# Kernel optimization log

Measured on AMD Instinct MI355X. Metric: run time of the kernel, lower is better.

The kernel has to match this reference:

```python
import jax, jax.numpy as jnp
import numpy as np
from jax import lax

B, C, H, W, E = 16, 256, 64, 64, 4
KH = KW = 3
EPS = 1e-5  # torch BatchNorm2d default


def conv2d(x, w, groups=1):
    # x: [N, Cin, H, W], w: [Cout, Cin/groups, KH, KW], stride 1, pad 1 (autopad for k=3)
    return lax.conv_general_dilated(
        x, w, window_strides=(1, 1), padding=[(1, 1), (1, 1)],
        dimension_numbers=('NCHW', 'OIHW', 'NCHW'),
        feature_group_count=groups)


def bn(t, g, b, m, v):
    # eval-mode batchnorm over channel dim of [N, C, H, W]
    scale = g / jnp.sqrt(v + EPS)
    return (t - m[:, None, None]) * scale[:, None, None] + b[:, None, None]


def silu(t):
    return t * jax.nn.sigmoid(t)


def setup_inputs() -> dict:
    key = jax.random.key(0)
    ks = jax.random.split(key, 8)
    s = lambda k, sh: jax.random.normal(k, sh, jnp.float32) * 0.05
    return {
        'x': jax.random.normal(ks[0], (B, C, H, W), jnp.float32),
        # cv1: Conv(c1, c_, 3) = conv(no bias) + BN + SiLU
        'w1': s(ks[1], (C, C, KH, KW)),
        'bn1_g': jnp.ones((C,), jnp.float32),
        'bn1_b': jnp.zeros((C,), jnp.float32),
        'bn1_m': s(ks[2], (C,)),
        'bn1_v': jnp.abs(s(ks[3], (C,))) + 1.0,
        # cv2: DynamicConv routing linear (C -> E experts)
        'wr': s(ks[4], (E, C)),
        'br': jnp.zeros((E,), jnp.float32),
        # CondConv2d expert weight bank: [E, Cout*Cin*KH*KW]
        'w_e': s(ks[5], (E, C * C * KH * KW)),
        # cv2 BatchNorm2d
        'bn2_g': jnp.ones((C,), jnp.float32),
        'bn2_b': jnp.zeros((C,), jnp.float32),
        'bn2_m': s(ks[6], (C,)),
        'bn2_v': jnp.abs(s(ks[7], (C,))) + 1.0,
    }


def reference(x, w1, bn1_g, bn1_b, bn1_m, bn1_v, wr, br, w_e,
              bn2_g, bn2_b, bn2_m, bn2_v):
    # cv1: standard YOLO Conv (3x3, pad 1) + BN + SiLU
    y = silu(bn(conv2d(x, w1), bn1_g, bn1_b, bn1_m, bn1_v))  # [B, C, H, W]

    # DynamicConv_Single: global-avg-pool routing -> sigmoid gates over experts
    pooled = y.mean(axis=(2, 3))                       # [B, C]
    routing = jax.nn.sigmoid(pooled @ wr.T + br)       # [B, E]

    # CondConv2d: per-sample expert-weighted kernel, applied via batch-as-groups
    kern = (routing @ w_e).reshape(B * C, C, KH, KW)   # [B*Cout, Cin, 3, 3]
    yc = conv2d(y.reshape(1, B * C, H, W), kern, groups=B).reshape(B, C, H, W)

    # cv2 BN + SiLU, then residual add (shortcut and c1 == c2)
    out = silu(bn(yc, bn2_g, bn2_b, bn2_m, bn2_v))
    return x + out


if __name__ == '__main__':
    o = reference(**setup_inputs())
    print(o.shape, o.dtype)
```

## Files before the change

### kernel.cpp

```cpp
#include <hip/hip_runtime.h>
#include <math.h>

typedef _Float16 h16;
typedef _Float16 half8 __attribute__((ext_vector_type(8)));
typedef float f32x4 __attribute__((ext_vector_type(4)));

#define BATCH 16
#define CH 256
#define EPSBN 1e-5f

constexpr size_t WE_STRIDE = (size_t)CH * CH * 9;
constexpr int RSTRIDE = 2120;
constexpr int BUFH    = 4 * RSTRIDE;

__device__ __forceinline__ float silu_(float v) {
    return v * (1.0f / (1.0f + __expf(-v)));
}

template<int MODE>
__global__ __launch_bounds__(256, 4)
void conv_mfma(const h16* __restrict__ xin,
               const h16* __restrict__ wt,
               const float* __restrict__ bng, const float* __restrict__ bnb,
               const float* __restrict__ bnm, const float* __restrict__ bnv,
               const float* __restrict__ resid,
               void* __restrict__ outv)
{
    __shared__ h16 xt[2 * BUFH];

    const int t = threadIdx.x;
    const int swz = (blockIdx.x & 7) * 128 + (blockIdx.x >> 3);
    const int bx  = swz & 31;
    const int gy  = swz >> 5;
    const int by  = gy & 1;
    const int bz  = gy >> 1;
    const int h0  = bx * 2;
    const int co0 = by * 128;
    const int wv   = t >> 6;
    const int ws   = wv >> 1;
    const int wc   = wv & 1;
    const int lane = t & 63;
    const int quad = lane >> 4;
    const int l15  = lane & 15;

    f32x4 acc[16];
    #pragma unroll
    for (int i = 0; i < 16; ++i) {
        f32x4 z = {0.f, 0.f, 0.f, 0.f};
        acc[i] = z;
    }

    const h16* wrow = wt + ((MODE == 1) ? (size_t)bz * 9 * 65536 : (size_t)0)
                         + ((size_t)(co0 + wc * 64 + l15) << 8)
                         + (size_t)(quad * 8);

    const h16* xb = xin + ((size_t)bz << 20);
    int goff[5];
    #pragma unroll
    for (int k = 0; k < 5; ++k) {
        int slot = k * 64 + lane;
        int row = slot / 66;
        int col = slot - row * 66;
        int gh = h0 - 1 + row, gw = col - 1;
        goff[k] = -1;
        if (slot < 264 && (unsigned)gh < 64u && (unsigned)gw < 64u)
            goff[k] = ((gh << 6) + gw) * 256 + wv * 8;
    }

    {
        half8 z = {0, 0, 0, 0, 0, 0, 0, 0};
        #pragma unroll
        for (int k = 0; k < 5; ++k) {
            int slot = k * 64 + lane;
            if (slot < 264 && goff[k] < 0) {
                *(half8*)(xt + wv * RSTRIDE + slot * 8) = z;
                *(half8*)(xt + BUFH + wv * RSTRIDE + slot * 8) = z;
            }
        }
    }

    auto stage = [&](int b, int ci0) {
        const h16* g = xb + ci0;
        #pragma unroll
        for (int k = 0; k < 5; ++k) {
            if (goff[k] >= 0)
                __builtin_amdgcn_global_load_lds(
                    (const __attribute__((address_space(1))) void*)(g + goff[k]),
                    (__attribute__((address_space(3))) void*)(xt + b * BUFH + wv * RSTRIDE + k * 512),
                    16, 0, 0);
        }
    };

    stage(0, 0);
    __syncthreads();

    for (int c = 0; c < 8; ++c) {
        if (c < 7) stage((c + 1) & 1, (c + 1) * 32);

        const h16* xq  = xt + (c & 1) * BUFH + quad * RSTRIDE + l15 * 8;
        const h16* wcp = wrow + c * 32;
        #pragma unroll
        for (int kh = 0; kh < 3; ++kh)
        #pragma unroll
        for (int kw = 0; kw < 3; ++kw) {
            const int tap = kh * 3 + kw;
            half8 wf[4], xf[4];
            #pragma unroll
            for (int f = 0; f < 4; ++f)
                wf[f] = *(const half8*)(wcp + (size_t)tap * 65536 + f * 4096);
            #pragma unroll
            for (int i = 0; i < 4; ++i)
                xf[i] = *(const half8*)(xq + ((ws + kh) * 66 + i * 16 + kw) * 8);
            if (MODE == 0) {
                #pragma unroll
                for (int i = 0; i < 4; ++i)
                    #pragma unroll
                    for (int j = 0; j < 4; ++j)
                        acc[i * 4 + j] = __builtin_amdgcn_mfma_f32_16x16x32_f16(
                            xf[i], wf[j], acc[i * 4 + j], 0, 0, 0);
            } else {
                #pragma unroll
                for (int i = 0; i < 4; ++i)
                    #pragma unroll
                    for (int j = 0; j < 4; ++j)
                        acc[i * 4 + j] = __builtin_amdgcn_mfma_f32_16x16x32_f16(
                            wf[i], xf[j], acc[i * 4 + j], 0, 0, 0);
            }
        }
        __syncthreads();
    }

    if (MODE == 0) {
        h16* yout = (h16*)outv;
        float sc[4], sh[4];
        #pragma unroll
        for (int j = 0; j < 4; ++j) {
            int cch = co0 + wc * 64 + j * 16 + l15;
            float s = bng[cch] * rsqrtf(bnv[cch] + EPSBN);
            sc[j] = s; sh[j] = bnb[cch] - bnm[cch] * s;
        }
        const int h = h0 + ws;
        #pragma unroll
        for (int i = 0; i < 4; ++i)
            #pragma unroll
            for (int r = 0; r < 4; ++r) {
                int w = i * 16 + quad * 4 + r;
                size_t base = (((size_t)(bz * 64 + h) << 6) + w) * 256
                            + co0 + wc * 64 + l15;
                #pragma unroll
                for (int j = 0; j < 4; ++j) {
                    float v = acc[i * 4 + j][r] * sc[j] + sh[j];
                    yout[base + j * 16] = (h16)silu_(v);
                }
            }
    } else {
        h16* ycp = (h16*)outv;
        const int h = h0 + ws;
        #pragma unroll
        for (int i = 0; i < 4; ++i) {
            float sc[4], sh[4];
            #pragma unroll
            for (int r = 0; r < 4; ++r) {
                int cch = co0 + wc * 64 + i * 16 + quad * 4 + r;
                float s = bng[cch] * rsqrtf(bnv[cch] + EPSBN);
                sc[r] = s; sh[r] = bnb[cch] - bnm[cch] * s;
            }
            #pragma unroll
            for (int j = 0; j < 4; ++j) {
                int w = j * 16 + l15;
                #pragma unroll
                for (int r = 0; r < 4; ++r) {
                    int cch = co0 + wc * 64 + i * 16 + quad * 4 + r;
                    size_t idx = ((size_t)(bz * CH + cch) << 12) + (h << 6) + w;
                    float v = acc[i * 4 + j][r] * sc[r] + sh[r];
                    ycp[idx] = (h16)silu_(v);
                }
            }
        }
    }
}

__global__ __launch_bounds__(256)
void finalize_kernel(const h16* __restrict__ yc, const float* __restrict__ x,
                     float* __restrict__ out) {
    const int total8 = BATCH * CH * 4096 / 8;
    int i = blockIdx.x * 256 + threadIdx.x;
    const int stride = gridDim.x * 256;
    for (; i < total8; i += stride) {
        half8 v = *(const half8*)(yc + (size_t)i * 8);
        const float4* xp = (const float4*)(x + (size_t)i * 8);
        float4 a = xp[0], b = xp[1];
        float4 o0, o1;
        o0.x = a.x + (float)v[0];
        o0.y = a.y + (float)v[1];
        o0.z = a.z + (float)v[2];
        o0.w = a.w + (float)v[3];
        o1.x = b.x + (float)v[4];
        o1.y = b.y + (float)v[5];
        o1.z = b.z + (float)v[6];
        o1.w = b.w + (float)v[7];
        float4* op = (float4*)(out + (size_t)i * 8);
        op[0] = o0;
        op[1] = o1;
    }
}

__global__ __launch_bounds__(256)
void prep_x(const float* __restrict__ x, h16* __restrict__ xh) {
    __shared__ float lt[64][65];
    int cg = blockIdx.x, h = blockIdx.y, b = blockIdx.z;
    int t = threadIdx.x;
    {
        int cl = t >> 2, wq = t & 3;
        const float4* src = (const float4*)(x + (((size_t)(b * CH + cg * 64 + cl)) << 12)
                                              + ((size_t)h << 6));
        #pragma unroll
        for (int k = 0; k < 4; ++k) {
            int w4 = wq + k * 4;
            float4 v = src[w4];
            lt[cl][w4 * 4 + 0] = v.x;
            lt[cl][w4 * 4 + 1] = v.y;
            lt[cl][w4 * 4 + 2] = v.z;
            lt[cl][w4 * 4 + 3] = v.w;
        }
    }
    __syncthreads();
    {
        int wl = t >> 2, cq = t & 3;
        half8 a2[2];
        h16* ap = (h16*)a2;
        #pragma unroll
        for (int m = 0; m < 16; ++m) ap[m] = (h16)lt[cq * 16 + m][wl];
        size_t base = ((((size_t)(b * 64 + h)) << 6) + wl) * 256 + cg * 64 + cq * 16;
        *(half8*)(xh + base)     = a2[0];
        *(half8*)(xh + base + 8) = a2[1];
    }
}

__global__ void prep_w1(const float* __restrict__ w1, h16* __restrict__ w1t) {
    int pair = blockIdx.x * 256 + threadIdx.x;
    #pragma unroll
    for (int tap = 0; tap < 9; ++tap)
        w1t[((size_t)tap << 16) + pair] = (h16)w1[(size_t)pair * 9 + tap];
}

__global__ __launch_bounds__(256)
void pool_kernel(const h16* __restrict__ y, float* __restrict__ part) {
    __shared__ float red[8][256];
    int slice = blockIdx.x, b = blockIdx.y;
    int t = threadIdx.x;
    int oct = t & 31, ss = t >> 5;
    float a[8];
    #pragma unroll
    for (int k = 0; k < 8; ++k) a[k] = 0.f;
    const h16* p = y + ((size_t)(b * 4096 + slice * 256 + ss)) * 256 + oct * 8;
    #pragma unroll 4
    for (int i = 0; i < 32; ++i) {
        half8 v = *(const half8*)(p + (size_t)i * 8 * 256);
        #pragma unroll
        for (int k = 0; k < 8; ++k) a[k] += (float)v[k];
    }
    #pragma unroll
    for (int k = 0; k < 8; ++k) red[ss][oct * 8 + k] = a[k];
    __syncthreads();
    float s = 0.f;
    #pragma unroll
    for (int q = 0; q < 8; ++q) s += red[q][t];
    part[((size_t)slice * BATCH + b) * 256 + t] = s;
}

__global__ void routing_kernel(const float* __restrict__ part,
                               const float* __restrict__ wr,
                               const float* __restrict__ br,
                               float* __restrict__ routing) {
    int t = threadIdx.x;
    if (t < 64) {
        int b = t >> 2, e = t & 3;
        float s = 0.f;
        for (int c = 0; c < 256; ++c) {
            float p = 0.f;
            for (int sl = 0; sl < 16; ++sl)
                p += part[((size_t)sl * BATCH + b) * 256 + c];
            s += p * wr[e * 256 + c];
        }
        s = s * (1.f / 4096.f) + br[e];
        routing[t] = 1.f / (1.f + __expf(-s));
    }
}

__global__ __launch_bounds__(256)
void kern_gen(const float* __restrict__ w_e,
              const float* __restrict__ routing,
              h16* __restrict__ wt2) {
    __shared__ float lw[4 * 2304];
    __shared__ float rsh[64];
    int t = threadIdx.x;
    int pair0 = blockIdx.x * 256;
    if (t < 64) rsh[t] = routing[t];
    #pragma unroll
    for (int e = 0; e < 4; ++e) {
        const float4* src = (const float4*)(w_e + (size_t)e * WE_STRIDE + (size_t)pair0 * 9);
        #pragma unroll
        for (int k = 0; k < 3; ++k) {
            int idx = t + k * 256;
            if (idx < 576) {
                float4 v = src[idx];
                float* d = &lw[e * 2304 + idx * 4];
                d[0] = v.x; d[1] = v.y; d[2] = v.z; d[3] = v.w;
            }
        }
    }
    __syncthreads();
    float wv[4][9];
    #pragma unroll
    for (int e = 0; e < 4; ++e)
        #pragma unroll
        for (int k = 0; k < 9; ++k)
            wv[e][k] = lw[e * 2304 + t * 9 + k];
    for (int b = 0; b < 16; ++b) {
        float r0 = rsh[b * 4 + 0], r1 = rsh[b * 4 + 1];
        float r2 = rsh[b * 4 + 2], r3 = rsh[b * 4 + 3];
        #pragma unroll
        for (int tap = 0; tap < 9; ++tap) {
            float s = r0 * wv[0][tap] + r1 * wv[1][tap]
                    + r2 * wv[2][tap] + r3 * wv[3][tap];
            wt2[((size_t)(b * 9 + tap) << 16) + pair0 + t] = (h16)s;
        }
    }
}

extern "C" void kernel_launch(void* const* d_in, const int* in_sizes, int n_in,
                              void* d_out, int out_size, void* d_ws, size_t ws_size,
                              hipStream_t stream) {
    const float* x    = (const float*)d_in[0];
    const float* w1   = (const float*)d_in[1];
    const float* bn1g = (const float*)d_in[2];
    const float* bn1b = (const float*)d_in[3];
    const float* bn1m = (const float*)d_in[4];
    const float* bn1v = (const float*)d_in[5];
    const float* wr   = (const float*)d_in[6];
    const float* br   = (const float*)d_in[7];
    const float* w_e  = (const float*)d_in[8];
    const float* bn2g = (const float*)d_in[9];
    const float* bn2b = (const float*)d_in[10];
    const float* bn2m = (const float*)d_in[11];
    const float* bn2v = (const float*)d_in[12];

    char* w = (char*)d_ws;
    h16*   xh      = (h16*)(w);
    h16*   y       = (h16*)(w + 33554432);
    h16*   w1t     = (h16*)(w + 67108864);
    h16*   wt2     = (h16*)(w + 68288512);
    float* part    = (float*)(w + 87162880);
    float* routing = (float*)(w + 87425024);

    prep_x<<<dim3(4, 64, BATCH), 256, 0, stream>>>(x, xh);
    prep_w1<<<dim3(256), 256, 0, stream>>>(w1, w1t);

    dim3 cgrid(1024);
    conv_mfma<0><<<cgrid, 256, 0, stream>>>(xh, w1t, bn1g, bn1b, bn1m, bn1v,
                                            nullptr, y);
    pool_kernel<<<dim3(16, BATCH), 256, 0, stream>>>(y, part);
    routing_kernel<<<dim3(1), 64, 0, stream>>>(part, wr, br, routing);
    kern_gen<<<dim3(256), 256, 0, stream>>>(w_e, routing, wt2);
    h16* yc = xh;
    conv_mfma<1><<<cgrid, 256, 0, stream>>>(y, wt2, bn2g, bn2b, bn2m, bn2v,
                                            nullptr, yc);
    finalize_kernel<<<dim3(2048), 256, 0, stream>>>(yc, x, (float*)d_out);
}
```

Baseline: 561.4 us.

## Enlarge conv tile to 4 rows x 128 channels per wave with double-buffered weight prefetch

```diff
diff --git a/kernel.cpp b/kernel.cpp
--- a/kernel.cpp
+++ b/kernel.cpp
@@ -10,15 +10,15 @@
 #define EPSBN 1e-5f
 
 constexpr size_t WE_STRIDE = (size_t)CH * CH * 9;
-constexpr int RSTRIDE = 2120;
-constexpr int BUFH    = 4 * RSTRIDE;
+constexpr int XREG  = 3176;
+constexpr int BUFH2 = 4 * XREG;
 
 __device__ __forceinline__ float silu_(float v) {
     return v * (1.0f / (1.0f + __expf(-v)));
 }
 
 template<int MODE>
-__global__ __launch_bounds__(256, 4)
+__global__ __launch_bounds__(256, 2)
 void conv_mfma(const h16* __restrict__ xin,
                const h16* __restrict__ wt,
                const float* __restrict__ bng, const float* __restrict__ bnb,
@@ -26,55 +26,54 @@
                const float* __restrict__ resid,
                void* __restrict__ outv)
 {
-    __shared__ h16 xt[2 * BUFH];
+    __shared__ h16 xt[2 * BUFH2];
 
     const int t = threadIdx.x;
-    const int swz = (blockIdx.x & 7) * 128 + (blockIdx.x >> 3);
-    const int bx  = swz & 31;
-    const int gy  = swz >> 5;
+    const int swz = (blockIdx.x & 7) * 64 + (blockIdx.x >> 3);
+    const int bx  = swz & 15;
+    const int gy  = swz >> 4;
     const int by  = gy & 1;
     const int bz  = gy >> 1;
-    const int h0  = bx * 2;
+    const int h0  = bx * 4;
     const int co0 = by * 128;
     const int wv   = t >> 6;
-    const int ws   = wv >> 1;
-    const int wc   = wv & 1;
+    const int ws   = wv;
     const int lane = t & 63;
     const int quad = lane >> 4;
     const int l15  = lane & 15;
 
-    f32x4 acc[16];
-    #pragma unroll
-    for (int i = 0; i < 16; ++i) {
+    f32x4 acc[32];
+    #pragma unroll
+    for (int i = 0; i < 32; ++i) {
         f32x4 z = {0.f, 0.f, 0.f, 0.f};
         acc[i] = z;
     }
 
     const h16* wrow = wt + ((MODE == 1) ? (size_t)bz * 9 * 65536 : (size_t)0)
-                         + ((size_t)(co0 + wc * 64 + l15) << 8)
+                         + ((size_t)(co0 + l15) << 8)
                          + (size_t)(quad * 8);
 
     const h16* xb = xin + ((size_t)bz << 20);
-    int goff[5];
-    #pragma unroll
-    for (int k = 0; k < 5; ++k) {
+    int goff[7];
+    #pragma unroll
+    for (int k = 0; k < 7; ++k) {
         int slot = k * 64 + lane;
         int row = slot / 66;
         int col = slot - row * 66;
         int gh = h0 - 1 + row, gw = col - 1;
         goff[k] = -1;
-        if (slot < 264 && (unsigned)gh < 64u && (unsigned)gw < 64u)
+        if (slot < 396 && (unsigned)gh < 64u && (unsigned)gw < 64u)
             goff[k] = ((gh << 6) + gw) * 256 + wv * 8;
     }
 
     {
         half8 z = {0, 0, 0, 0, 0, 0, 0, 0};
         #pragma unroll
-        for (int k = 0; k < 5; ++k) {
+        for (int k = 0; k < 7; ++k) {
             int slot = k * 64 + lane;
-            if (slot < 264 && goff[k] < 0) {
-                *(half8*)(xt + wv * RSTRIDE + slot * 8) = z;
-                *(half8*)(xt + BUFH + wv * RSTRIDE + slot * 8) = z;
+            if (slot < 396 && goff[k] < 0) {
+                *(half8*)(xt + wv * XREG + slot * 8) = z;
+                *(half8*)(xt + BUFH2 + wv * XREG + slot * 8) = z;
             }
         }
     }
@@ -82,11 +81,11 @@
     auto stage = [&](int b, int ci0) {
         const h16* g = xb + ci0;
         #pragma unroll
-        for (int k = 0; k < 5; ++k) {
+        for (int k = 0; k < 7; ++k) {
             if (goff[k] >= 0)
                 __builtin_amdgcn_global_load_lds(
                     (const __attribute__((address_space(1))) void*)(g + goff[k]),
-                    (__attribute__((address_space(3))) void*)(xt + b * BUFH + wv * RSTRIDE + k * 512),
+                    (__attribute__((address_space(3))) void*)(xt + b * BUFH2 + wv * XREG + k * 512),
                     16, 0, 0);
         }
     };
@@ -94,20 +93,28 @@
     stage(0, 0);
     __syncthreads();
 
+    #pragma unroll 1
     for (int c = 0; c < 8; ++c) {
+        const h16* wc = wrow + c * 32;
+        half8 wfb[2][8];
+        #pragma unroll
+        for (int f = 0; f < 8; ++f)
+            wfb[0][f] = *(const half8*)(wc + (size_t)f * 4096);
+
         if (c < 7) stage((c + 1) & 1, (c + 1) * 32);
 
-        const h16* xq  = xt + (c & 1) * BUFH + quad * RSTRIDE + l15 * 8;
-        const h16* wcp = wrow + c * 32;
-        #pragma unroll
-        for (int kh = 0; kh < 3; ++kh)
-        #pragma unroll
-        for (int kw = 0; kw < 3; ++kw) {
-            const int tap = kh * 3 + kw;
-            half8 wf[4], xf[4];
-            #pragma unroll
-            for (int f = 0; f < 4; ++f)
-                wf[f] = *(const half8*)(wcp + (size_t)tap * 65536 + f * 4096);
+        const h16* xq = xt + (c & 1) * BUFH2 + quad * XREG + l15 * 8;
+        #pragma unroll
+        for (int tap = 0; tap < 9; ++tap) {
+            const int cur = tap & 1, nxt = cur ^ 1;
+            if (tap < 8) {
+                #pragma unroll
+                for (int f = 0; f < 8; ++f)
+                    wfb[nxt][f] = *(const half8*)(wc + (size_t)(tap + 1) * 65536
+                                                     + (size_t)f * 4096);
+            }
+            const int kh = tap / 3, kw = tap - kh * 3;
+            half8 xf[4];
             #pragma unroll
             for (int i = 0; i < 4; ++i)
                 xf[i] = *(const half8*)(xq + ((ws + kh) * 66 + i * 16 + kw) * 8);
@@ -115,16 +122,16 @@
                 #pragma unroll
                 for (int i = 0; i < 4; ++i)
                     #pragma unroll
-                    for (int j = 0; j < 4; ++j)
-                        acc[i * 4 + j] = __builtin_amdgcn_mfma_f32_16x16x32_f16(
-                            xf[i], wf[j], acc[i * 4 + j], 0, 0, 0);
+                    for (int j = 0; j < 8; ++j)
+                        acc[i * 8 + j] = __builtin_amdgcn_mfma_f32_16x16x32_f16(
+                            xf[i], wfb[cur][j], acc[i * 8 + j], 0, 0, 0);
             } else {
                 #pragma unroll
                 for (int i = 0; i < 4; ++i)
                     #pragma unroll
-                    for (int j = 0; j < 4; ++j)
-                        acc[i * 4 + j] = __builtin_amdgcn_mfma_f32_16x16x32_f16(
-                            wf[i], xf[j], acc[i * 4 + j], 0, 0, 0);
+                    for (int j = 0; j < 8; ++j)
+                        acc[i * 8 + j] = __builtin_amdgcn_mfma_f32_16x16x32_f16(
+                            wfb[cur][j], xf[i], acc[i * 8 + j], 0, 0, 0);
             }
         }
         __syncthreads();
@@ -132,10 +139,10 @@
 
     if (MODE == 0) {
         h16* yout = (h16*)outv;
-        float sc[4], sh[4];
-        #pragma unroll
-        for (int j = 0; j < 4; ++j) {
-            int cch = co0 + wc * 64 + j * 16 + l15;
+        float sc[8], sh[8];
+        #pragma unroll
+        for (int j = 0; j < 8; ++j) {
+            int cch = co0 + j * 16 + l15;
             float s = bng[cch] * rsqrtf(bnv[cch] + EPSBN);
             sc[j] = s; sh[j] = bnb[cch] - bnm[cch] * s;
         }
@@ -146,10 +153,10 @@
             for (int r = 0; r < 4; ++r) {
                 int w = i * 16 + quad * 4 + r;
                 size_t base = (((size_t)(bz * 64 + h) << 6) + w) * 256
-                            + co0 + wc * 64 + l15;
-                #pragma unroll
-                for (int j = 0; j < 4; ++j) {
-                    float v = acc[i * 4 + j][r] * sc[j] + sh[j];
+                            + co0 + l15;
+                #pragma unroll
+                for (int j = 0; j < 8; ++j) {
+                    float v = acc[i * 8 + j][r] * sc[j] + sh[j];
                     yout[base + j * 16] = (h16)silu_(v);
                 }
             }
@@ -157,22 +164,22 @@
         h16* ycp = (h16*)outv;
         const int h = h0 + ws;
         #pragma unroll
-        for (int i = 0; i < 4; ++i) {
+        for (int j = 0; j < 8; ++j) {
             float sc[4], sh[4];
             #pragma unroll
             for (int r = 0; r < 4; ++r) {
-                int cch = co0 + wc * 64 + i * 16 + quad * 4 + r;
+                int cch = co0 + j * 16 + quad * 4 + r;
                 float s = bng[cch] * rsqrtf(bnv[cch] + EPSBN);
                 sc[r] = s; sh[r] = bnb[cch] - bnm[cch] * s;
             }
             #pragma unroll
-            for (int j = 0; j < 4; ++j) {
-                int w = j * 16 + l15;
+            for (int i = 0; i < 4; ++i) {
+                int w = i * 16 + l15;
                 #pragma unroll
                 for (int r = 0; r < 4; ++r) {
-                    int cch = co0 + wc * 64 + i * 16 + quad * 4 + r;
+                    int cch = co0 + j * 16 + quad * 4 + r;
                     size_t idx = ((size_t)(bz * CH + cch) << 12) + (h << 6) + w;
-                    float v = acc[i * 4 + j][r] * sc[r] + sh[r];
+                    float v = acc[i * 8 + j][r] * sc[r] + sh[r];
                     ycp[idx] = (h16)silu_(v);
                 }
             }
@@ -357,7 +364,7 @@
     prep_x<<<dim3(4, 64, BATCH), 256, 0, stream>>>(x, xh);
     prep_w1<<<dim3(256), 256, 0, stream>>>(w1, w1t);
 
-    dim3 cgrid(1024);
+    dim3 cgrid(512);
     conv_mfma<0><<<cgrid, 256, 0, stream>>>(xh, w1t, bn1g, bn1b, bn1m, bn1v,
                                             nullptr, y);
     pool_kernel<<<dim3(16, BATCH), 256, 0, stream>>>(y, part);
```

Measured after the change: 556.1 us. About the same (-1.0%).

## Replace LDS-staged conv tiles with single-wave direct-global-load blocks

Applied to the files above, without the earlier changes.

```diff
diff --git a/kernel.cpp b/kernel.cpp
--- a/kernel.cpp
+++ b/kernel.cpp
@@ -10,15 +10,13 @@
 #define EPSBN 1e-5f
 
 constexpr size_t WE_STRIDE = (size_t)CH * CH * 9;
-constexpr int RSTRIDE = 2120;
-constexpr int BUFH    = 4 * RSTRIDE;
 
 __device__ __forceinline__ float silu_(float v) {
     return v * (1.0f / (1.0f + __expf(-v)));
 }
 
 template<int MODE>
-__global__ __launch_bounds__(256, 4)
+__global__ __launch_bounds__(64, 3)
 void conv_mfma(const h16* __restrict__ xin,
                const h16* __restrict__ wt,
                const float* __restrict__ bng, const float* __restrict__ bnb,
@@ -26,22 +24,14 @@
                const float* __restrict__ resid,
                void* __restrict__ outv)
 {
-    __shared__ h16 xt[2 * BUFH];
-
-    const int t = threadIdx.x;
-    const int swz = (blockIdx.x & 7) * 128 + (blockIdx.x >> 3);
-    const int bx  = swz & 31;
-    const int gy  = swz >> 5;
-    const int by  = gy & 1;
-    const int bz  = gy >> 1;
-    const int h0  = bx * 2;
-    const int co0 = by * 128;
-    const int wv   = t >> 6;
-    const int ws   = wv >> 1;
-    const int wc   = wv & 1;
-    const int lane = t & 63;
+    const int lane = threadIdx.x;
     const int quad = lane >> 4;
     const int l15  = lane & 15;
+    const int swz = (blockIdx.x & 7) * 512 + (blockIdx.x >> 3);
+    const int h   = swz & 63;
+    const int cog = (swz >> 6) & 3;
+    const int b   = swz >> 8;
+    const int co0 = cog * 64;
 
     f32x4 acc[16];
     #pragma unroll
@@ -50,129 +40,105 @@
         acc[i] = z;
     }
 
-    const h16* wrow = wt + ((MODE == 1) ? (size_t)bz * 9 * 65536 : (size_t)0)
-                         + ((size_t)(co0 + wc * 64 + l15) << 8)
-                         + (size_t)(quad * 8);
-
-    const h16* xb = xin + ((size_t)bz << 20);
-    int goff[5];
-    #pragma unroll
-    for (int k = 0; k < 5; ++k) {
-        int slot = k * 64 + lane;
-        int row = slot / 66;
-        int col = slot - row * 66;
-        int gh = h0 - 1 + row, gw = col - 1;
-        goff[k] = -1;
-        if (slot < 264 && (unsigned)gh < 64u && (unsigned)gw < 64u)
-            goff[k] = ((gh << 6) + gw) * 256 + wv * 8;
-    }
-
-    {
-        half8 z = {0, 0, 0, 0, 0, 0, 0, 0};
-        #pragma unroll
-        for (int k = 0; k < 5; ++k) {
-            int slot = k * 64 + lane;
-            if (slot < 264 && goff[k] < 0) {
-                *(half8*)(xt + wv * RSTRIDE + slot * 8) = z;
-                *(half8*)(xt + BUFH + wv * RSTRIDE + slot * 8) = z;
-            }
-        }
-    }
-
-    auto stage = [&](int b, int ci0) {
-        const h16* g = xb + ci0;
-        #pragma unroll
-        for (int k = 0; k < 5; ++k) {
-            if (goff[k] >= 0)
-                __builtin_amdgcn_global_load_lds(
-                    (const __attribute__((address_space(1))) void*)(g + goff[k]),
-                    (__attribute__((address_space(3))) void*)(xt + b * BUFH + wv * RSTRIDE + k * 512),
-                    16, 0, 0);
-        }
-    };
-
-    stage(0, 0);
-    __syncthreads();
-
-    for (int c = 0; c < 8; ++c) {
-        if (c < 7) stage((c + 1) & 1, (c + 1) * 32);
-
-        const h16* xq  = xt + (c & 1) * BUFH + quad * RSTRIDE + l15 * 8;
-        const h16* wcp = wrow + c * 32;
-        #pragma unroll
-        for (int kh = 0; kh < 3; ++kh)
-        #pragma unroll
-        for (int kw = 0; kw < 3; ++kw) {
-            const int tap = kh * 3 + kw;
+    const h16* wbase = wt + ((MODE == 1) ? (size_t)b * 9 * 65536 : (size_t)0)
+                          + ((size_t)(co0 + l15) << 8)
+                          + (size_t)(quad * 8);
+    const h16* xbase = xin + ((size_t)b << 20);
+
+    #pragma unroll 1
+    for (int tap = 0; tap < 9; ++tap) {
+        const int kh = tap / 3, kw = tap - kh * 3;
+        const int r  = h + kh - 1;
+        if ((unsigned)r >= 64u) continue;
+
+        const h16* wp[4];
+        #pragma unroll
+        for (int f = 0; f < 4; ++f)
+            wp[f] = wbase + (size_t)tap * 65536 + f * 16 * 256;
+
+        const h16* xr = xbase + (((size_t)r << 6) << 8);
+        const h16* xp[4];
+        int inv[4];
+        #pragma unroll
+        for (int i = 0; i < 4; ++i) {
+            int wr_ = i * 16 + l15 + kw - 1;
+            int inb = ((unsigned)wr_ < 64u);
+            int wcl = inb ? wr_ : (wr_ < 0 ? 0 : 63);
+            inv[i] = !inb;
+            xp[i] = xr + wcl * 256 + quad * 8;
+        }
+
+        #pragma unroll
+        for (int c = 0; c < 8; ++c) {
             half8 wf[4], xf[4];
             #pragma unroll
             for (int f = 0; f < 4; ++f)
-                wf[f] = *(const half8*)(wcp + (size_t)tap * 65536 + f * 4096);
-            #pragma unroll
-            for (int i = 0; i < 4; ++i)
-                xf[i] = *(const half8*)(xq + ((ws + kh) * 66 + i * 16 + kw) * 8);
+                wf[f] = *(const half8*)(wp[f] + c * 32);
+            #pragma unroll
+            for (int i = 0; i < 4; ++i) {
+                half8 v = *(const half8*)(xp[i] + c * 32);
+                if (inv[i]) { half8 z = {0, 0, 0, 0, 0, 0, 0, 0}; v = z; }
+                xf[i] = v;
+            }
             if (MODE == 0) {
                 #pragma unroll
                 for (int i = 0; i < 4; ++i)
                     #pragma unroll
-                    for (int j = 0; j < 4; ++j)
-                        acc[i * 4 + j] = __builtin_amdgcn_mfma_f32_16x16x32_f16(
-                            xf[i], wf[j], acc[i * 4 + j], 0, 0, 0);
+                    for (int f = 0; f < 4; ++f)
+                        acc[i * 4 + f] = __builtin_amdgcn_mfma_f32_16x16x32_f16(
+                            xf[i], wf[f], acc[i * 4 + f], 0, 0, 0);
             } else {
                 #pragma unroll
                 for (int i = 0; i < 4; ++i)
                     #pragma unroll
-                    for (int j = 0; j < 4; ++j)
-                        acc[i * 4 + j] = __builtin_amdgcn_mfma_f32_16x16x32_f16(
-                            wf[i], xf[j], acc[i * 4 + j], 0, 0, 0);
-            }
-        }
-        __syncthreads();
+                    for (int f = 0; f < 4; ++f)
+                        acc[i * 4 + f] = __builtin_amdgcn_mfma_f32_16x16x32_f16(
+                            wf[f], xf[i], acc[i * 4 + f], 0, 0, 0);
+            }
+        }
     }
 
     if (MODE == 0) {
         h16* yout = (h16*)outv;
         float sc[4], sh[4];
         #pragma unroll
-        for (int j = 0; j < 4; ++j) {
-            int cch = co0 + wc * 64 + j * 16 + l15;
+        for (int f = 0; f < 4; ++f) {
+            int cch = co0 + f * 16 + l15;
             float s = bng[cch] * rsqrtf(bnv[cch] + EPSBN);
-            sc[j] = s; sh[j] = bnb[cch] - bnm[cch] * s;
-        }
-        const int h = h0 + ws;
+            sc[f] = s; sh[f] = bnb[cch] - bnm[cch] * s;
+        }
         #pragma unroll
         for (int i = 0; i < 4; ++i)
             #pragma unroll
             for (int r = 0; r < 4; ++r) {
                 int w = i * 16 + quad * 4 + r;
-                size_t base = (((size_t)(bz * 64 + h) << 6) + w) * 256
-                            + co0 + wc * 64 + l15;
+                size_t base = (((size_t)(b * 64 + h) << 6) + w) * 256
+                            + co0 + l15;
                 #pragma unroll
-                for (int j = 0; j < 4; ++j) {
-                    float v = acc[i * 4 + j][r] * sc[j] + sh[j];
-                    yout[base + j * 16] = (h16)silu_(v);
+                for (int f = 0; f < 4; ++f) {
+                    float v = acc[i * 4 + f][r] * sc[f] + sh[f];
+                    yout[base + f * 16] = (h16)silu_(v);
                 }
             }
     } else {
         h16* ycp = (h16*)outv;
-        const int h = h0 + ws;
-        #pragma unroll
-        for (int i = 0; i < 4; ++i) {
+        #pragma unroll
+        for (int f = 0; f < 4; ++f) {
             float sc[4], sh[4];
             #pragma unroll
             for (int r = 0; r < 4; ++r) {
-                int cch = co0 + wc * 64 + i * 16 + quad * 4 + r;
+                int cch = co0 + f * 16 + quad * 4 + r;
                 float s = bng[cch] * rsqrtf(bnv[cch] + EPSBN);
                 sc[r] = s; sh[r] = bnb[cch] - bnm[cch] * s;
             }
             #pragma unroll
-            for (int j = 0; j < 4; ++j) {
-                int w = j * 16 + l15;
+            for (int i = 0; i < 4; ++i) {
+                int w = i * 16 + l15;
                 #pragma unroll
                 for (int r = 0; r < 4; ++r) {
-                    int cch = co0 + wc * 64 + i * 16 + quad * 4 + r;
-                    size_t idx = ((size_t)(bz * CH + cch) << 12) + (h << 6) + w;
-                    float v = acc[i * 4 + j][r] * sc[r] + sh[r];
+                    int cch = co0 + f * 16 + quad * 4 + r;
+                    size_t idx = ((size_t)(b * CH + cch) << 12) + (h << 6) + w;
+                    float v = acc[i * 4 + f][r] * sc[r] + sh[r];
                     ycp[idx] = (h16)silu_(v);
                 }
             }
@@ -357,14 +323,14 @@
     prep_x<<<dim3(4, 64, BATCH), 256, 0, stream>>>(x, xh);
     prep_w1<<<dim3(256), 256, 0, stream>>>(w1, w1t);
 
-    dim3 cgrid(1024);
-    conv_mfma<0><<<cgrid, 256, 0, stream>>>(xh, w1t, bn1g, bn1b, bn1m, bn1v,
-                                            nullptr, y);
+    dim3 cgrid(4096);
+    conv_mfma<0><<<cgrid, 64, 0, stream>>>(xh, w1t, bn1g, bn1b, bn1m, bn1v,
+                                           nullptr, y);
     pool_kernel<<<dim3(16, BATCH), 256, 0, stream>>>(y, part);
     routing_kernel<<<dim3(1), 64, 0, stream>>>(part, wr, br, routing);
     kern_gen<<<dim3(256), 256, 0, stream>>>(w_e, routing, wt2);
     h16* yc = xh;
-    conv_mfma<1><<<cgrid, 256, 0, stream>>>(y, wt2, bn2g, bn2b, bn2m, bn2v,
-                                            nullptr, yc);
+    conv_mfma<1><<<cgrid, 64, 0, stream>>>(y, wt2, bn2g, bn2b, bn2m, bn2v,
+                                           nullptr, yc);
     finalize_kernel<<<dim3(2048), 256, 0, stream>>>(yc, x, (float*)d_out);
 }
```

After: 944.1 us. 68.2% more time.
